# Performance work log

Hardware: AMD Instinct MI355X
Metric: run time of the kernel (lower is better)

The kernel has to match this reference:

```python
import jax, jax.numpy as jnp
from jax import lax
import numpy as np

GROUPS = 128
EPS = 1e-7


def setup_inputs() -> dict:
    key = jax.random.key(0)
    k1, k2, k3, k4 = jax.random.split(key, 4)
    B, Cin, Cout, H, W, K = 8, 256, 256, 128, 128, 3
    return {
        "x": jax.random.normal(k1, (B, Cin, H, W), jnp.float32),
        "dw_kernels": jax.random.normal(k2, (B, Cout, Cin // GROUPS, K, K), jnp.float32) * 0.1,
        "pw_kernels": jax.random.normal(k3, (B, Cout, Cout // GROUPS, 1, 1), jnp.float32) * 0.1,
        "biases": jax.random.normal(k4, (B, Cout), jnp.float32) * 0.1,
    }


def _normalize(x):
    # torch.std uses Bessel's correction (divide by N-1)
    mean = jnp.mean(x, axis=(2, 3), keepdims=True)
    n = x.shape[2] * x.shape[3]
    var = jnp.sum((x - mean) ** 2, axis=(2, 3), keepdims=True) / (n - 1)
    std = jnp.sqrt(var) + EPS
    return (x - mean) / std


def _adaconv(x, dw_kernels, pw_kernels, biases):
    B, Cin, H, W = x.shape
    Cout = dw_kernels.shape[1]
    K = dw_kernels.shape[-1]
    pad = (K - 1) // 2

    xn = _normalize(x)
    xp = jnp.pad(xn, ((0, 0), (0, 0), (pad, pad), (pad, pad)))

    # per-sample grouped spatial conv via vmap over batch
    def dw_one(xi, wi):
        # xi: [Cin, H+2p, W+2p], wi: [Cout, Cin//G, K, K]
        return lax.conv_general_dilated(
            xi[None], wi, window_strides=(1, 1), padding="VALID",
            feature_group_count=GROUPS)[0]

    dw_out = jax.vmap(dw_one)(xp, dw_kernels)  # [B, Cout, H, W]

    # grouped 1x1 conv as a per-group small matmul
    cg = Cout // GROUPS
    dwg = dw_out.reshape(B, GROUPS, cg, H, W)
    pwg = pw_kernels.reshape(B, GROUPS, cg, cg)  # [b, g, out_sub, in_sub]
    out = jnp.einsum("bgoi,bgihw->bgohw", pwg, dwg).reshape(B, Cout, H, W)
    return out + biases[:, :, None, None]


def reference(x, dw_kernels, pw_kernels, biases):
    return _adaconv(x, dw_kernels, pw_kernels, biases)
```

## Files before the change

### kernel.cpp

```cpp
#include <hip/hip_runtime.h>
#include <math.h>

#define BATCH 8
#define CH    256
#define HH    128
#define WW    128
#define HW    (HH*WW)
#define NGRP  128
#define CPG   2
#define EPS   1e-7f

__global__ __launch_bounds__(256) void stats_kernel(
    const float* __restrict__ x, float* __restrict__ mean_o, float* __restrict__ rstd_o)
{
    const int c = blockIdx.x;
    const float4* p = (const float4*)(x + (size_t)c * HW);
    float s = 0.f, ss = 0.f;
    for (int i = threadIdx.x; i < HW/4; i += 256) {
        float4 v = p[i];
        s  += v.x + v.y + v.z + v.w;
        ss += v.x*v.x + v.y*v.y + v.z*v.z + v.w*v.w;
    }
    #pragma unroll
    for (int off = 32; off > 0; off >>= 1) {
        s  += __shfl_down(s,  off);
        ss += __shfl_down(ss, off);
    }
    __shared__ float ls[4], lss[4];
    const int wave = threadIdx.x >> 6;
    if ((threadIdx.x & 63) == 0) { ls[wave] = s; lss[wave] = ss; }
    __syncthreads();
    if (threadIdx.x == 0) {
        s  = ls[0]  + ls[1]  + ls[2]  + ls[3];
        ss = lss[0] + lss[1] + lss[2] + lss[3];
        const float m   = s * (1.0f / (float)HW);
        float var = (ss - s * m) * (1.0f / (float)(HW - 1));
        var = fmaxf(var, 0.0f);
        const float sd = sqrtf(var) + EPS;
        mean_o[c] = m;
        rstd_o[c] = 1.0f / sd;
    }
}

#define TH 16
#define TW 64

__global__ __launch_bounds__(256) void adaconv_kernel(
    const float* __restrict__ x,
    const float* __restrict__ dwk,
    const float* __restrict__ pwk,
    const float* __restrict__ bias,
    const float* __restrict__ mean_i,
    const float* __restrict__ rstd_i,
    float* __restrict__ out)
{
    const int b  = blockIdx.z;
    const int g  = blockIdx.y;
    const int th0 = (blockIdx.x >> 1) * TH;
    const int tw0 = (blockIdx.x & 1)  * TW;

    const int c0  = g * CPG;
    const int bc0 = b * CH + c0;

    __shared__ float xs[CPG][TH + 2][TW + 2];

    const float m0 = mean_i[bc0],     r0 = rstd_i[bc0];
    const float m1 = mean_i[bc0 + 1], r1 = rstd_i[bc0 + 1];
    const float* xb = x + (size_t)bc0 * HW;

    const int NE = CPG * (TH + 2) * (TW + 2);
    for (int e = threadIdx.x; e < NE; e += 256) {
        const int c   = e / ((TH + 2) * (TW + 2));
        const int rem = e - c * ((TH + 2) * (TW + 2));
        const int r   = rem / (TW + 2);
        const int col = rem - r * (TW + 2);
        const int gh = th0 + r - 1;
        const int gw = tw0 + col - 1;
        float v = 0.0f;
        if (gh >= 0 && gh < HH && gw >= 0 && gw < WW) {
            v = xb[c * HW + gh * WW + gw];
            v = (v - (c ? m1 : m0)) * (c ? r1 : r0);
        }
        ((float*)xs)[e] = v;
    }

    float wdw[2][2][9];
    #pragma unroll
    for (int co = 0; co < 2; ++co)
        #pragma unroll
        for (int ci = 0; ci < 2; ++ci)
            #pragma unroll
            for (int k = 0; k < 9; ++k)
                wdw[co][ci][k] = dwk[(((size_t)(bc0 + co)) * 2 + ci) * 9 + k];

    const float p00 = pwk[(size_t)(bc0 + 0) * 2 + 0];
    const float p01 = pwk[(size_t)(bc0 + 0) * 2 + 1];
    const float p10 = pwk[(size_t)(bc0 + 1) * 2 + 0];
    const float p11 = pwk[(size_t)(bc0 + 1) * 2 + 1];
    const float bb0 = bias[bc0], bb1 = bias[bc0 + 1];

    __syncthreads();

    const int tx = threadIdx.x & 63;
    const int rg = threadIdx.x >> 6;
    float* outb = out + (size_t)bc0 * HW;

    #pragma unroll
    for (int j = 0; j < 4; ++j) {
        const int r = rg * 4 + j;
        float d0 = 0.f, d1 = 0.f;
        #pragma unroll
        for (int ci = 0; ci < 2; ++ci) {
            #pragma unroll
            for (int ky = 0; ky < 3; ++ky) {
                #pragma unroll
                for (int kx = 0; kx < 3; ++kx) {
                    const float v = xs[ci][r + ky][tx + kx];
                    d0 = fmaf(v, wdw[0][ci][ky * 3 + kx], d0);
                    d1 = fmaf(v, wdw[1][ci][ky * 3 + kx], d1);
                }
            }
        }
        const int gh = th0 + r;
        const int gw = tw0 + tx;
        outb[gh * WW + gw]      = fmaf(p00, d0, fmaf(p01, d1, bb0));
        outb[HW + gh * WW + gw] = fmaf(p10, d0, fmaf(p11, d1, bb1));
    }
}

extern "C" void kernel_launch(void* const* d_in, const int* in_sizes, int n_in,
                              void* d_out, int out_size, void* d_ws, size_t ws_size,
                              hipStream_t stream)
{
    const float* x    = (const float*)d_in[0];
    const float* dwk  = (const float*)d_in[1];
    const float* pwk  = (const float*)d_in[2];
    const float* bias = (const float*)d_in[3];
    float* out  = (float*)d_out;

    float* mean_b = (float*)d_ws;
    float* rstd_b = mean_b + BATCH * CH;

    stats_kernel<<<BATCH * CH, 256, 0, stream>>>(x, mean_b, rstd_b);

    dim3 grid((HH / TH) * (WW / TW), NGRP, BATCH);
    adaconv_kernel<<<grid, 256, 0, stream>>>(x, dwk, pwk, bias, mean_b, rstd_b, out);
}
```

Measured before the change: 282.1 us.

## Fold pointwise weights into depthwise taps and register-block full-width row tiles

The depthwise and 2x2 pointwise weights are pre-multiplied, so each output channel becomes a single 3x3x2 conv and the separate pointwise step goes away. Tiles now span the full 128-column width, which removes horizontal halos. The input is loaded and normalized with float4 loads. Each thread computes 2 rows by 4 columns by 2 channels from reused row vectors and writes float4 stores. This cuts the address arithmetic, scalar LDS traffic and global store count, at the cost of more registers and fewer blocks.

```diff
diff --git a/kernel.cpp b/kernel.cpp
--- a/kernel.cpp
+++ b/kernel.cpp
@@ -16,6 +16,7 @@
     const int c = blockIdx.x;
     const float4* p = (const float4*)(x + (size_t)c * HW);
     float s = 0.f, ss = 0.f;
+    #pragma unroll 4
     for (int i = threadIdx.x; i < HW/4; i += 256) {
         float4 v = p[i];
         s  += v.x + v.y + v.z + v.w;
@@ -33,7 +34,7 @@
     if (threadIdx.x == 0) {
         s  = ls[0]  + ls[1]  + ls[2]  + ls[3];
         ss = lss[0] + lss[1] + lss[2] + lss[3];
-        const float m   = s * (1.0f / (float)HW);
+        const float m = s * (1.0f / (float)HW);
         float var = (ss - s * m) * (1.0f / (float)(HW - 1));
         var = fmaxf(var, 0.0f);
         const float sd = sqrtf(var) + EPS;
@@ -43,7 +44,7 @@
 }
 
 #define TH 16
-#define TW 64
+#define XSS 136
 
 __global__ __launch_bounds__(256) void adaconv_kernel(
     const float* __restrict__ x,
@@ -54,77 +55,106 @@
     const float* __restrict__ rstd_i,
     float* __restrict__ out)
 {
-    const int b  = blockIdx.z;
-    const int g  = blockIdx.y;
-    const int th0 = (blockIdx.x >> 1) * TH;
-    const int tw0 = (blockIdx.x & 1)  * TW;
+    const int b   = blockIdx.z;
+    const int g   = blockIdx.y;
+    const int th0 = blockIdx.x * TH;
+    const int bc0 = b * CH + g * CPG;
+    const int tid = threadIdx.x;
 
-    const int c0  = g * CPG;
-    const int bc0 = b * CH + c0;
+    __shared__ float xs[CPG][TH + 2][XSS];
 
-    __shared__ float xs[CPG][TH + 2][TW + 2];
-
-    const float m0 = mean_i[bc0],     r0 = rstd_i[bc0];
-    const float m1 = mean_i[bc0 + 1], r1 = rstd_i[bc0 + 1];
+    const float r0s = rstd_i[bc0],     m0 = mean_i[bc0];
+    const float r1s = rstd_i[bc0 + 1], m1 = mean_i[bc0 + 1];
+    const float nm0 = -m0 * r0s, nm1 = -m1 * r1s;
     const float* xb = x + (size_t)bc0 * HW;
 
-    const int NE = CPG * (TH + 2) * (TW + 2);
-    for (int e = threadIdx.x; e < NE; e += 256) {
-        const int c   = e / ((TH + 2) * (TW + 2));
-        const int rem = e - c * ((TH + 2) * (TW + 2));
-        const int r   = rem / (TW + 2);
-        const int col = rem - r * (TW + 2);
-        const int gh = th0 + r - 1;
-        const int gw = tw0 + col - 1;
-        float v = 0.0f;
-        if (gh >= 0 && gh < HH && gw >= 0 && gw < WW) {
-            v = xb[c * HW + gh * WW + gw];
-            v = (v - (c ? m1 : m0)) * (c ? r1 : r0);
-        }
-        ((float*)xs)[e] = v;
+    if (tid < CPG * (TH + 2)) {
+        const int ci  = tid / (TH + 2);
+        const int row = tid - ci * (TH + 2);
+        xs[ci][row][3]   = 0.f;
+        xs[ci][row][132] = 0.f;
     }
 
-    float wdw[2][2][9];
-    #pragma unroll
-    for (int co = 0; co < 2; ++co)
-        #pragma unroll
-        for (int ci = 0; ci < 2; ++ci)
-            #pragma unroll
-            for (int k = 0; k < 9; ++k)
-                wdw[co][ci][k] = dwk[(((size_t)(bc0 + co)) * 2 + ci) * 9 + k];
+    for (int e = tid; e < CPG * (TH + 2) * 32; e += 256) {
+        const int ci  = e / ((TH + 2) * 32);
+        const int rem = e - ci * ((TH + 2) * 32);
+        const int row = rem >> 5;
+        const int c4  = rem & 31;
+        const int gh  = th0 + row - 1;
+        float4 v = make_float4(0.f, 0.f, 0.f, 0.f);
+        if (gh >= 0 && gh < HH) {
+            v = *(const float4*)(xb + (size_t)ci * HW + gh * WW + (c4 << 2));
+            const float sc = ci ? r1s : r0s;
+            const float ad = ci ? nm1 : nm0;
+            v.x = fmaf(v.x, sc, ad); v.y = fmaf(v.y, sc, ad);
+            v.z = fmaf(v.z, sc, ad); v.w = fmaf(v.w, sc, ad);
+        }
+        *(float4*)&xs[ci][row][4 + (c4 << 2)] = v;
+    }
 
     const float p00 = pwk[(size_t)(bc0 + 0) * 2 + 0];
     const float p01 = pwk[(size_t)(bc0 + 0) * 2 + 1];
     const float p10 = pwk[(size_t)(bc0 + 1) * 2 + 0];
     const float p11 = pwk[(size_t)(bc0 + 1) * 2 + 1];
+    const float* dwb = dwk + (size_t)bc0 * 18;
+    float we[2][2][9];
+    #pragma unroll
+    for (int ci = 0; ci < 2; ++ci)
+        #pragma unroll
+        for (int k = 0; k < 9; ++k) {
+            const float w0 = dwb[ci * 9 + k];
+            const float w1 = dwb[18 + ci * 9 + k];
+            we[0][ci][k] = fmaf(p00, w0, p01 * w1);
+            we[1][ci][k] = fmaf(p10, w0, p11 * w1);
+        }
     const float bb0 = bias[bc0], bb1 = bias[bc0 + 1];
 
     __syncthreads();
 
-    const int tx = threadIdx.x & 63;
-    const int rg = threadIdx.x >> 6;
-    float* outb = out + (size_t)bc0 * HW;
+    const int c0    = (tid & 31) << 2;
+    const int rbase = (tid >> 5) << 1;
+
+    float acc[2][2][4];
+    #pragma unroll
+    for (int o = 0; o < 2; ++o)
+        #pragma unroll
+        for (int cc = 0; cc < 4; ++cc) { acc[o][0][cc] = bb0; acc[o][1][cc] = bb1; }
 
     #pragma unroll
-    for (int j = 0; j < 4; ++j) {
-        const int r = rg * 4 + j;
-        float d0 = 0.f, d1 = 0.f;
+    for (int r = 0; r < 4; ++r) {
         #pragma unroll
         for (int ci = 0; ci < 2; ++ci) {
+            const float* rowp = &xs[ci][rbase + r][0];
+            const float2 L = *(const float2*)(rowp + c0 + 2);
+            const float4 M = *(const float4*)(rowp + c0 + 4);
+            const float2 R = *(const float2*)(rowp + c0 + 8);
+            const float xv[6] = { L.y, M.x, M.y, M.z, M.w, R.x };
             #pragma unroll
-            for (int ky = 0; ky < 3; ++ky) {
+            for (int o = 0; o < 2; ++o) {
+                const int ky = r - o;
+                if (ky < 0 || ky > 2) continue;
                 #pragma unroll
-                for (int kx = 0; kx < 3; ++kx) {
-                    const float v = xs[ci][r + ky][tx + kx];
-                    d0 = fmaf(v, wdw[0][ci][ky * 3 + kx], d0);
-                    d1 = fmaf(v, wdw[1][ci][ky * 3 + kx], d1);
-                }
+                for (int ch = 0; ch < 2; ++ch)
+                    #pragma unroll
+                    for (int cc = 0; cc < 4; ++cc)
+                        #pragma unroll
+                        for (int kx = 0; kx < 3; ++kx)
+                            acc[o][ch][cc] = fmaf(we[ch][ci][ky * 3 + kx],
+                                                  xv[cc + kx], acc[o][ch][cc]);
             }
         }
-        const int gh = th0 + r;
-        const int gw = tw0 + tx;
-        outb[gh * WW + gw]      = fmaf(p00, d0, fmaf(p01, d1, bb0));
-        outb[HW + gh * WW + gw] = fmaf(p10, d0, fmaf(p11, d1, bb1));
+    }
+
+    float* outb = out + (size_t)bc0 * HW;
+    #pragma unroll
+    for (int o = 0; o < 2; ++o) {
+        const int gr = th0 + rbase + o;
+        #pragma unroll
+        for (int ch = 0; ch < 2; ++ch) {
+            const float4 vv = make_float4(acc[o][ch][0], acc[o][ch][1],
+                                          acc[o][ch][2], acc[o][ch][3]);
+            *(float4*)(outb + (size_t)ch * HW + gr * WW + c0) = vv;
+        }
     }
 }
 
@@ -136,13 +166,13 @@
     const float* dwk  = (const float*)d_in[1];
     const float* pwk  = (const float*)d_in[2];
     const float* bias = (const float*)d_in[3];
-    float* out  = (float*)d_out;
+    float* out = (float*)d_out;
 
     float* mean_b = (float*)d_ws;
     float* rstd_b = mean_b + BATCH * CH;
 
     stats_kernel<<<BATCH * CH, 256, 0, stream>>>(x, mean_b, rstd_b);
 
-    dim3 grid((HH / TH) * (WW / TW), NGRP, BATCH);
+    dim3 grid(HH / TH, NGRP, BATCH);
     adaconv_kernel<<<grid, 256, 0, stream>>>(x, dwk, pwk, bias, mean_b, rstd_b, out);
 }
```

Result: faster. 274.8 us (-2.6%).
